# Kernel tuning notes

Measured on AMD Instinct MI355X. Metric: run time of the kernel, lower is better.

Reference implementation:

```python
import jax, jax.numpy as jnp
import numpy as np

NUM_NOD = 6
MAX_PREV = 5
NUM_EDGE = 20  # (1+5)*5//2 + 5*(6-5)
D = 1024
H = 8
LN_EPS = 1e-6


def setup_inputs() -> dict:
    key = jax.random.key(0)
    ks = jax.random.split(key, 12)
    B, S = 8, 1024
    scale = 1.0 / np.sqrt(D)
    return {
        "inputs": jax.random.normal(ks[0], (B, S, D), jnp.float32),
        "ew": jax.random.uniform(ks[1], (NUM_NOD, 3), jnp.float32),
        "act_w": jax.random.uniform(ks[2], (NUM_NOD,), jnp.float32),
        "We": jax.random.normal(ks[3], (NUM_EDGE, D, D), jnp.float32) * scale,
        "be": jnp.zeros((NUM_EDGE, D), jnp.float32),
        "Wq": jax.random.normal(ks[4], (NUM_NOD, D, D), jnp.float32) * scale,
        "Wk": jax.random.normal(ks[5], (NUM_NOD, D, D), jnp.float32) * scale,
        "Wv": jax.random.normal(ks[6], (NUM_NOD, D, D), jnp.float32) * scale,
        "Wo": jax.random.normal(ks[7], (NUM_NOD, D, D), jnp.float32) * scale,
        "ln_g": jnp.ones((D,), jnp.float32),
        "ln_b": jnp.zeros((D,), jnp.float32),
    }


def _layernorm(x, g, b):
    mu = jnp.mean(x, axis=-1, keepdims=True)
    var = jnp.mean(jnp.square(x - mu), axis=-1, keepdims=True)
    return (x - mu) * jax.lax.rsqrt(var + LN_EPS) * g + b


def _mha(q, k, v, wq, wk, wv, wo):
    B, S, d = q.shape
    dh = d // H
    qh = (q @ wq).reshape(B, S, H, dh)
    kh = (k @ wk).reshape(B, S, H, dh)
    vh = (v @ wv).reshape(B, S, H, dh)
    scores = jnp.einsum("bqhd,bkhd->bhqk", qh, kh) / jnp.sqrt(jnp.asarray(dh, q.dtype))
    attn = jax.nn.softmax(scores, axis=-1)
    ctx = jnp.einsum("bhqk,bkhd->bqhd", attn, vh).reshape(B, S, d)
    return ctx @ wo


def reference(inputs, ew, act_w, We, be, Wq, Wk, Wv, Wo, ln_g, ln_b):
    # Fixed (deterministic) routing: node act = attention (q,k,v) for all nodes.
    # Edge op = linear (sel_ope 3). q from node c-1, k from earliest visible node,
    # v from the middle of the visible window; gated by Gumbel weights ew/act_w.
    nodes = {-1: inputs}
    lind = 0
    for c in range(NUM_NOD):
        nsrc = min(c + 1, MAX_PREV)
        snode = c - nsrc
        eq, ek, ev = lind + nsrc - 1, lind, lind + nsrc // 2
        in_q, in_k, in_v = c - 1, snode, snode + nsrc // 2
        q = ew[c, 0] * (nodes[in_q] @ We[eq] + be[eq])
        k = ew[c, 1] * (nodes[in_k] @ We[ek] + be[ek])
        v = ew[c, 2] * (nodes[in_v] @ We[ev] + be[ev])
        o = _mha(q, k, v, Wq[c], Wk[c], Wv[c], Wo[c])
        nodes[c] = act_w[c] * o + q  # gated attention + residual
        lind += nsrc
    # only node 5 is unconsumed under this routing
    out = nodes[NUM_NOD - 1]
    return _layernorm(out, ln_g, ln_b)
```

## Files before the change

kernel.cpp:

```cpp
#include <hip/hip_runtime.h>
#include <stdint.h>

#define DD 1024
#define MM 8192

typedef unsigned short u16;
typedef __attribute__((ext_vector_type(8))) short s16x8;
typedef __attribute__((ext_vector_type(4))) short s16x4;
typedef __attribute__((ext_vector_type(8))) __bf16 bf16x8;
typedef __attribute__((ext_vector_type(4))) float f32x4;

__device__ inline u16 f2bf(float f) {
  uint32_t u = __builtin_bit_cast(uint32_t, f);
  u += 0x7fffu + ((u >> 16) & 1u);
  return (u16)(u >> 16);
}
__device__ inline u16 f2bf_rn(float f) {
  return __builtin_bit_cast(u16, (__bf16)f);
}
__device__ inline float bf2f(u16 h) {
  return __builtin_bit_cast(float, (uint32_t)h << 16);
}
__device__ inline f32x4 mfma32(s16x8 a, s16x8 b, f32x4 c) {
  return __builtin_amdgcn_mfma_f32_16x16x32_bf16(
      __builtin_bit_cast(bf16x8, a), __builtin_bit_cast(bf16x8, b), c, 0, 0, 0);
}

struct CvtJobs { const float* p[23]; u16* d[23]; };
__global__ __launch_bounds__(256) void k_cvtN(CvtJobs cs) {
  int z = blockIdx.y;
  const float4* p = (const float4*)cs.p[z];
  u16* out = cs.d[z];
  int i = blockIdx.x * 256 + threadIdx.x;
  float4 a = p[2 * i], b = p[2 * i + 1];
  union { s16x8 v; u16 u[8]; } r;
  r.u[0] = f2bf(a.x); r.u[1] = f2bf(a.y); r.u[2] = f2bf(a.z); r.u[3] = f2bf(a.w);
  r.u[4] = f2bf(b.x); r.u[5] = f2bf(b.y); r.u[6] = f2bf(b.z); r.u[7] = f2bf(b.w);
  ((s16x8*)out)[i] = r.v;
}

struct WSrcs { const float* p[18]; };
__global__ __launch_bounds__(256) void k_wtransN(WSrcs ws, u16* __restrict__ pool) {
  __shared__ u16 t[32][33];
  int m = blockIdx.z;
  const float* src = ws.p[m];
  u16* dst = pool + (size_t)m * DD * DD;
  int c0 = blockIdx.x * 32, r0 = blockIdx.y * 32;
  int tx = threadIdx.x, ty = threadIdx.y;
  #pragma unroll
  for (int j = 0; j < 4; ++j)
    t[ty + j * 8][tx] = f2bf(src[(size_t)(r0 + ty + j * 8) * DD + c0 + tx]);
  __syncthreads();
  #pragma unroll
  for (int j = 0; j < 4; ++j)
    dst[(size_t)(c0 + ty + j * 8) * DD + r0 + tx] = t[tx][ty + j * 8];
}

struct BiasArgs { const float* be[18]; };
__global__ __launch_bounds__(256) void k_biasN(BiasArgs ba, const u16* __restrict__ wt,
                                               float* __restrict__ outv) {
  int z = blockIdx.y, n = blockIdx.x * 256 + threadIdx.x;
  const u16* row = wt + (size_t)z * DD * DD + (size_t)n * DD;
  const float* be = ba.be[z];
  float acc = 0.0f;
  for (int k8 = 0; k8 < DD / 8; ++k8) {
    s16x8 w = *(const s16x8*)(row + k8 * 8);
    const float4* bp = (const float4*)(be + k8 * 8);
    float4 b0 = bp[0], b1 = bp[1];
    acc += b0.x * bf2f((u16)w[0]) + b0.y * bf2f((u16)w[1]) +
           b0.z * bf2f((u16)w[2]) + b0.w * bf2f((u16)w[3]) +
           b1.x * bf2f((u16)w[4]) + b1.y * bf2f((u16)w[5]) +
           b1.z * bf2f((u16)w[6]) + b1.w * bf2f((u16)w[7]);
  }
  outv[(size_t)z * DD + n] = acc;
}

struct CombArgs { const u16* a[18]; const u16* b[18]; u16* cbase; };
__global__ __launch_bounds__(256, 2) void k_gemmC(CombArgs ca) {
  const u16* A = ca.a[blockIdx.z];
  const u16* Bt = ca.b[blockIdx.z];
  u16* C = ca.cbase + (size_t)blockIdx.z * DD * DD;
  __shared__ u16 As[128 * 64];
  __shared__ u16 Bs[128 * 64];
  const int tid = threadIdx.x;
  const int lane = tid & 63, wave = tid >> 6;
  const int g = lane >> 4, r15 = lane & 15;
  const int m0 = blockIdx.x * 128, n0 = blockIdx.y * 128;
  const int wm = (wave >> 1) * 64, wn = (wave & 1) * 64;
  f32x4 acc[4][4] = {};
  for (int kt = 0; kt < 16; ++kt) {
    const int k0 = kt * 64;
    __syncthreads();
    #pragma unroll
    for (int i = 0; i < 4; ++i) {
      int c = tid + i * 256;
      int row = c >> 3, kc = (c & 7) ^ (row & 7);
      __builtin_amdgcn_global_load_lds(
          (__attribute__((address_space(1))) void*)(A + (size_t)(m0 + row) * DD + k0 + kc * 8),
          (__attribute__((address_space(3))) void*)(As + c * 8), 16, 0, 0);
    }
    #pragma unroll
    for (int i = 0; i < 4; ++i) {
      int c = tid + i * 256;
      int row = c >> 3, kc = (c & 7) ^ (row & 7);
      __builtin_amdgcn_global_load_lds(
          (__attribute__((address_space(1))) void*)(Bt + (size_t)(n0 + row) * DD + k0 + kc * 8),
          (__attribute__((address_space(3))) void*)(Bs + c * 8), 16, 0, 0);
    }
    __syncthreads();
    #pragma unroll
    for (int ks = 0; ks < 2; ++ks) {
      s16x8 af[4], bfr[4];
      #pragma unroll
      for (int f = 0; f < 4; ++f) {
        int row = wm + f * 16 + r15;
        int kc = (ks * 4 + g) ^ (row & 7);
        af[f] = *(const s16x8*)(As + row * 64 + kc * 8);
        int rowb = wn + f * 16 + r15;
        int kcb = (ks * 4 + g) ^ (rowb & 7);
        bfr[f] = *(const s16x8*)(Bs + rowb * 64 + kcb * 8);
      }
      #pragma unroll
      for (int fm = 0; fm < 4; ++fm)
        #pragma unroll
        for (int fn = 0; fn < 4; ++fn)
          acc[fm][fn] = mfma32(af[fm], bfr[fn], acc[fm][fn]);
    }
  }
  #pragma unroll
  for (int fm = 0; fm < 4; ++fm)
    #pragma unroll
    for (int fn = 0; fn < 4; ++fn) {
      int col = n0 + wn + fn * 16 + r15;
      #pragma unroll
      for (int j = 0; j < 4; ++j) {
        int row = m0 + wm + fm * 16 + g * 4 + j;
        C[(size_t)row * DD + col] = f2bf(acc[fm][fn][j]);
      }
    }
}

struct GemmJob {
  const u16* A; const u16* Bt; const float* bias; const u16* resid;
  float* f32out;
  u16* out0; const float* s0p; float s0c;
  u16* out1; const float* s1p;
  u16* out2; const float* s2p;
  u16* vtout;
};
struct GemmBatch { GemmJob j[3]; };

__global__ __launch_bounds__(256, 2) void k_gemmN(GemmBatch gb) {
  const GemmJob jb = gb.j[blockIdx.z];
  __shared__ u16 As[128 * 64];
  __shared__ u16 Bs[128 * 64];
  const int tid = threadIdx.x;
  const int lane = tid & 63, wave = tid >> 6;
  const int g = lane >> 4, r15 = lane & 15;
  const int m0 = blockIdx.x * 128, n0 = blockIdx.y * 128;
  const int wm = (wave >> 1) * 64, wn = (wave & 1) * 64;
  f32x4 acc[4][4] = {};
  for (int kt = 0; kt < 16; ++kt) {
    const int k0 = kt * 64;
    __syncthreads();
    #pragma unroll
    for (int i = 0; i < 4; ++i) {
      int c = tid + i * 256;
      int row = c >> 3, kc = (c & 7) ^ (row & 7);
      __builtin_amdgcn_global_load_lds(
          (__attribute__((address_space(1))) void*)(jb.A + (size_t)(m0 + row) * DD + k0 + kc * 8),
          (__attribute__((address_space(3))) void*)(As + c * 8), 16, 0, 0);
    }
    #pragma unroll
    for (int i = 0; i < 4; ++i) {
      int c = tid + i * 256;
      int row = c >> 3, kc = (c & 7) ^ (row & 7);
      __builtin_amdgcn_global_load_lds(
          (__attribute__((address_space(1))) void*)(jb.Bt + (size_t)(n0 + row) * DD + k0 + kc * 8),
          (__attribute__((address_space(3))) void*)(Bs + c * 8), 16, 0, 0);
    }
    __syncthreads();
    #pragma unroll
    for (int ks = 0; ks < 2; ++ks) {
      s16x8 af[4], bfr[4];
      #pragma unroll
      for (int f = 0; f < 4; ++f) {
        int row = wm + f * 16 + r15;
        int kc = (ks * 4 + g) ^ (row & 7);
        af[f] = *(const s16x8*)(As + row * 64 + kc * 8);
        int rowb = wn + f * 16 + r15;
        int kcb = (ks * 4 + g) ^ (rowb & 7);
        bfr[f] = *(const s16x8*)(Bs + rowb * 64 + kcb * 8);
      }
      #pragma unroll
      for (int fm = 0; fm < 4; ++fm)
        #pragma unroll
        for (int fn = 0; fn < 4; ++fn)
          acc[fm][fn] = mfma32(af[fm], bfr[fn], acc[fm][fn]);
    }
  }
  const float s0 = jb.s0c * (jb.s0p ? jb.s0p[0] : 1.0f);
  if (jb.vtout) {
    #pragma unroll
    for (int fm = 0; fm < 4; ++fm) {
      #pragma unroll
      for (int fn = 0; fn < 4; ++fn) {
        int col = n0 + wn + fn * 16 + r15;
        float bcol = jb.bias ? jb.bias[col] : 0.0f;
        int row0 = m0 + wm + fm * 16 + g * 4;
        int b_ = row0 >> 10, h_ = col >> 7, d_ = col & 127, s_ = row0 & 1023;
        union { s16x4 v; u16 u[4]; } q4;
        #pragma unroll
        for (int j = 0; j < 4; ++j) q4.u[j] = f2bf(s0 * (acc[fm][fn][j] + bcol));
        *(s16x4*)(jb.vtout + (((size_t)(b_ * 8 + h_) * 128 + d_) << 10) + s_) = q4.v;
      }
    }
    return;
  }
  const float s1 = (jb.s1p ? jb.s1p[0] : 1.0f);
  const float s2 = (jb.s2p ? jb.s2p[0] : 1.0f);
  #pragma unroll
  for (int fm = 0; fm < 4; ++fm) {
    #pragma unroll
    for (int fn = 0; fn < 4; ++fn) {
      int col = n0 + wn + fn * 16 + r15;
      float bcol = jb.bias ? jb.bias[col] : 0.0f;
      #pragma unroll
      for (int j = 0; j < 4; ++j) {
        int row = m0 + wm + fm * 16 + g * 4 + j;
        size_t idx = (size_t)row * DD + col;
        float v = acc[fm][fn][j] + bcol;
        float v0 = s0 * v + (jb.resid ? bf2f(jb.resid[idx]) : 0.0f);
        if (jb.out0) jb.out0[idx] = f2bf(v0);
        if (jb.f32out) jb.f32out[idx] = v0;
        if (jb.out1) jb.out1[idx] = f2bf(s1 * v);
        if (jb.out2) jb.out2[idx] = f2bf(s2 * v);
      }
    }
  }
}

__global__ __launch_bounds__(256, 2) void k_attn(
    const u16* __restrict__ qp, const u16* __restrict__ kp,
    const u16* __restrict__ vt, u16* __restrict__ ctx) {
  __shared__ u16 Ks[2][64 * 128];
  __shared__ u16 Vs[128 * 72];
  const int lin = blockIdx.y * gridDim.x + blockIdx.x;
  const int m = lin >> 3;
  const int bh = (lin & 7) * 8 + (m & 7);
  const int q0 = (m >> 3) * 128;
  const int b = bh >> 3, h = bh & 7;
  const int tid = threadIdx.x, lane = tid & 63, wave = tid >> 6;
  const int g = lane >> 4, r15 = lane & 15;
  s16x8 qf[2][4];
  #pragma unroll
  for (int qg = 0; qg < 2; ++qg) {
    const u16* qb = qp + (size_t)(b * 1024 + q0 + wave * 32 + qg * 16 + r15) * DD + h * 128;
    #pragma unroll
    for (int kk = 0; kk < 4; ++kk) qf[qg][kk] = *(const s16x8*)(qb + kk * 32 + g * 8);
  }
  f32x4 o0[8] = {}, o1[8] = {};
  float lps0 = 0.0f, lps1 = 0.0f;
  const u16* kpb = kp + (size_t)b * 1024 * DD + h * 128;
  const u16* vtb = vt + (size_t)bh * 128 * 1024;

  s16x8 vreg[4];
  auto stageK = [&](int t, int buf) {
    #pragma unroll
    for (int i = 0; i < 4; ++i) {
      int c = tid + i * 256;
      int row = c >> 4, kc = (c & 15) ^ (row & 7);
      __builtin_amdgcn_global_load_lds(
          (__attribute__((address_space(1))) void*)(kpb + (size_t)(t * 64 + row) * DD + kc * 8),
          (__attribute__((address_space(3))) void*)(Ks[buf] + c * 8), 16, 0, 0);
    }
  };
  auto loadV = [&](int t) {
    #pragma unroll
    for (int i = 0; i < 4; ++i) {
      int c = tid + i * 256;
      int row = c >> 3, kc = c & 7;
      vreg[i] = *(const s16x8*)(vtb + (size_t)row * 1024 + t * 64 + kc * 8);
    }
  };
  auto writeV = [&]() {
    #pragma unroll
    for (int i = 0; i < 4; ++i) {
      int c = tid + i * 256;
      int row = c >> 3, kc = c & 7;
      *(s16x8*)(Vs + row * 72 + kc * 8) = vreg[i];
    }
  };

  stageK(0, 0);
  loadV(0);
  writeV();
  __syncthreads();

  union pk_t { s16x8 v; u16 u[8]; };
  for (int t = 0; t < 16; ++t) {
    const int cur = t & 1;
    if (t < 15) {
      stageK(t + 1, cur ^ 1);
      loadV(t + 1);
    }
    f32x4 s0[4] = {}, s1[4] = {};
    __builtin_amdgcn_s_setprio(1);
    #pragma unroll
    for (int sub = 0; sub < 4; ++sub) {
      const int krow = sub * 16 + r15;
      #pragma unroll
      for (int kk = 0; kk < 4; ++kk) {
        int slot = (kk * 4 + g) ^ (krow & 7);
        s16x8 kf = *(const s16x8*)(Ks[cur] + krow * 128 + slot * 8);
        s0[sub] = mfma32(kf, qf[0][kk], s0[sub]);
        s1[sub] = mfma32(kf, qf[1][kk], s1[sub]);
      }
    }
    __builtin_amdgcn_s_setprio(0);
    pk_t pa0[2], pa1[2];
    #pragma unroll
    for (int sub = 0; sub < 4; ++sub)
      #pragma unroll
      for (int j = 0; j < 4; ++j) {
        float pe = exp2f(s0[sub][j] - 16.0f);
        lps0 += pe;
        pa0[sub >> 1].u[(sub & 1) * 4 + j] = f2bf_rn(pe);
      }
    #pragma unroll
    for (int sub = 0; sub < 4; ++sub)
      #pragma unroll
      for (int j = 0; j < 4; ++j) {
        float pe = exp2f(s1[sub][j] - 16.0f);
        lps1 += pe;
        pa1[sub >> 1].u[(sub & 1) * 4 + j] = f2bf_rn(pe);
      }
    __builtin_amdgcn_s_setprio(1);
    #pragma unroll
    for (int p01 = 0; p01 < 2; ++p01) {
      #pragma unroll
      for (int dt = 0; dt < 8; ++dt) {
        union { s16x8 v; s16x4 h[2]; } vv;
        const u16* vbase = Vs + (dt * 16 + r15) * 72 + p01 * 32 + g * 4;
        vv.h[0] = *(const s16x4*)(vbase);
        vv.h[1] = *(const s16x4*)(vbase + 16);
        o0[dt] = mfma32(pa0[p01].v, vv.v, o0[dt]);
        o1[dt] = mfma32(pa1[p01].v, vv.v, o1[dt]);
      }
    }
    __builtin_amdgcn_s_setprio(0);
    __syncthreads();
    if (t < 15) {
      writeV();
      __syncthreads();
    }
  }
  lps0 += __shfl_xor(lps0, 16);
  lps0 += __shfl_xor(lps0, 32);
  lps1 += __shfl_xor(lps1, 16);
  lps1 += __shfl_xor(lps1, 32);
  {
    float inv = 1.0f / lps0;
    #pragma unroll
    for (int j = 0; j < 4; ++j) {
      float cj = __shfl(inv, (lane & 48) + g * 4 + j);
      size_t row = (size_t)(b * 1024 + q0 + wave * 32 + g * 4 + j);
      #pragma unroll
      for (int dt = 0; dt < 8; ++dt)
        ctx[row * DD + h * 128 + dt * 16 + r15] = f2bf(o0[dt][j] * cj);
    }
  }
  {
    float inv = 1.0f / lps1;
    #pragma unroll
    for (int j = 0; j < 4; ++j) {
      float cj = __shfl(inv, (lane & 48) + g * 4 + j);
      size_t row = (size_t)(b * 1024 + q0 + wave * 32 + 16 + g * 4 + j);
      #pragma unroll
      for (int dt = 0; dt < 8; ++dt)
        ctx[row * DD + h * 128 + dt * 16 + r15] = f2bf(o1[dt][j] * cj);
    }
  }
}

__global__ __launch_bounds__(256) void k_ln(const float* __restrict__ x,
                                            const float* __restrict__ gam,
                                            const float* __restrict__ bet,
                                            float* __restrict__ out) {
  __shared__ float red[8];
  const int row = blockIdx.x, tid = threadIdx.x, lane = tid & 63, wave = tid >> 6;
  const float4 v = ((const float4*)(x + (size_t)row * DD))[tid];
  float s = v.x + v.y + v.z + v.w;
  #pragma unroll
  for (int m = 1; m < 64; m <<= 1) s += __shfl_xor(s, m);
  if (lane == 0) red[wave] = s;
  __syncthreads();
  float mu = (red[0] + red[1] + red[2] + red[3]) * (1.0f / DD);
  float dx = v.x - mu, dy = v.y - mu, dz = v.z - mu, dw = v.w - mu;
  float q = dx * dx + dy * dy + dz * dz + dw * dw;
  #pragma unroll
  for (int m = 1; m < 64; m <<= 1) q += __shfl_xor(q, m);
  if (lane == 0) red[wave + 4] = q;
  __syncthreads();
  float var = (red[4] + red[5] + red[6] + red[7]) * (1.0f / DD);
  float inv = rsqrtf(var + 1e-6f);
  const float4 gv = ((const float4*)gam)[tid];
  const float4 bv = ((const float4*)bet)[tid];
  float4 r;
  r.x = dx * inv * gv.x + bv.x;
  r.y = dy * inv * gv.y + bv.y;
  r.z = dz * inv * gv.z + bv.z;
  r.w = dw * inv * gv.w + bv.w;
  ((float4*)(out + (size_t)row * DD))[tid] = r;
}

extern "C" void kernel_launch(void* const* d_in, const int* in_sizes, int n_in,
                              void* d_out, int out_size, void* d_ws, size_t ws_size,
                              hipStream_t stream) {
  const float* inputs = (const float*)d_in[0];
  const float* ew     = (const float*)d_in[1];
  const float* act_w  = (const float*)d_in[2];
  const float* We     = (const float*)d_in[3];
  const float* be     = (const float*)d_in[4];
  const float* Wq     = (const float*)d_in[5];
  const float* Wk     = (const float*)d_in[6];
  const float* Wv     = (const float*)d_in[7];
  const float* Wo     = (const float*)d_in[8];
  const float* ln_g   = (const float*)d_in[9];
  const float* ln_b   = (const float*)d_in[10];
  float* out = (float*)d_out;

  uint8_t* w = (uint8_t*)d_ws;
  size_t off = 0;
  auto alloc = [&](size_t bytes) {
    uint8_t* p = w + off;
    off += (bytes + 255) & ~(size_t)255;
    return p;
  };
  const size_t XB = (size_t)MM * DD * 2;
  const size_t WB = (size_t)DD * DD * 2;
  const size_t XBu = (size_t)MM * DD;
  const size_t WBu = (size_t)DD * DD;

  u16* Xbuf[5];
  for (int i = 0; i < 5; ++i) Xbuf[i] = (u16*)alloc(XB);
  u16* Comb  = (u16*)alloc(18 * WB);
  u16* rot   = (u16*)alloc(4 * WB);
  float* biasv = (float*)alloc(18 * DD * 4);
  u16* S     = (u16*)alloc(5 * XB);
  if (off > ws_size) {
    (void)hipMemsetAsync(d_out, 0x7F, (size_t)out_size * 4, stream);
    return;
  }
  u16* Xb[6] = {Xbuf[0], Xbuf[1], Xbuf[2], Xbuf[3], Xbuf[4], Xbuf[0]};
  u16* qb = S, * ctxb = S + XBu, * qpb = S + 2 * XBu, * kpb = S + 3 * XBu,
     * vtb = S + 4 * XBu;
  float* n5 = (float*)qpb;
  u16* stP = S;
  u16* stW = S + 18 * WBu;

  struct Node { int sq, eq, sk, ek, sv, ev; };
  static const Node route[6] = {
      {-1, 0, -1, 0, -1, 0},
      {0, 2, -1, 1, 0, 2},
      {1, 5, -1, 3, 0, 4},
      {2, 9, -1, 6, 1, 8},
      {3, 14, -1, 10, 1, 12},
      {4, 19, 0, 15, 2, 17},
  };
  const float QS = 1.4426950408889634f * 0.088388347648318433f;

  int emap[20]; for (int i = 0; i < 20; ++i) emap[i] = -1;
  int uniq[20]; int nu = 0;
  for (int c = 0; c < 6; ++c) {
    int es[3] = {route[c].eq, route[c].ek, route[c].ev};
    for (int t = 0; t < 3; ++t)
      if (emap[es[t]] < 0) { emap[es[t]] = nu; uniq[nu++] = es[t]; }
  }

  CvtJobs cv;
  for (int j = 0; j < nu; ++j) { cv.p[j] = We + (size_t)uniq[j] * WBu; cv.d[j] = stW + (size_t)j * WBu; }
  for (int j = 0; j < 8; ++j)  { cv.p[nu + j] = inputs + (size_t)j * WBu; cv.d[nu + j] = Xb[0] + (size_t)j * WBu; }
  k_cvtN<<<dim3(512, nu + 8), 256, 0, stream>>>(cv);
  WSrcs w18;
  for (int c = 0; c < 6; ++c) {
    w18.p[c * 3 + 0] = Wq + (size_t)c * WBu;
    w18.p[c * 3 + 1] = Wk + (size_t)c * WBu;
    w18.p[c * 3 + 2] = Wv + (size_t)c * WBu;
  }
  k_wtransN<<<dim3(32, 32, 18), dim3(32, 8), 0, stream>>>(w18, stP);
  CombArgs ca;
  BiasArgs ba;
  for (int c = 0; c < 6; ++c) {
    int es[3] = {route[c].eq, route[c].ek, route[c].ev};
    for (int t = 0; t < 3; ++t) {
      int i = c * 3 + t;
      ca.a[i] = stP + (size_t)i * WBu;
      ca.b[i] = stW + (size_t)emap[es[t]] * WBu;
      ba.be[i] = be + (size_t)es[t] * DD;
    }
  }
  ca.cbase = Comb;
  k_gemmC<<<dim3(8, 8, 18), 256, 0, stream>>>(ca);
  k_biasN<<<dim3(4, 18), 256, 0, stream>>>(ba, stP, biasv);

  GemmJob oprojPrev{};
  for (int c = 0; c < 6; ++c) {
    const Node& nd = route[c];
    u16* qeT = rot + (size_t)(c & 1) * 2 * WBu;
    u16* WoT = qeT + WBu;

    GemmJob kap = {Xb[nd.sk + 1], Comb + (size_t)(c * 3 + 1) * WBu,
                   biasv + (size_t)(c * 3 + 1) * DD, nullptr, nullptr,
                   kpb, ew + 3 * c + 1, 1.0f,
                   nullptr, nullptr, nullptr, nullptr, nullptr};
    GemmJob vap = {Xb[nd.sv + 1], Comb + (size_t)(c * 3 + 2) * WBu,
                   biasv + (size_t)(c * 3 + 2) * DD, nullptr, nullptr,
                   nullptr, ew + 3 * c + 2, 1.0f,
                   nullptr, nullptr, nullptr, nullptr, vtb};
    GemmJob qed = {Xb[nd.sq + 1], qeT, be + (size_t)nd.eq * DD, nullptr, nullptr,
                   qb, ew + 3 * c + 0, 1.0f,
                   nullptr, nullptr, nullptr, nullptr, nullptr};
    GemmJob qap = {Xb[nd.sq + 1], Comb + (size_t)(c * 3 + 0) * WBu,
                   biasv + (size_t)(c * 3 + 0) * DD, nullptr, nullptr,
                   qpb, ew + 3 * c + 0, QS,
                   nullptr, nullptr, nullptr, nullptr, nullptr};

    GemmBatch A{};
    int za = 0;
    if (c >= 1) A.j[za++] = oprojPrev;
    A.j[za++] = kap;
    if (c != 1) A.j[za++] = vap;
    k_gemmN<<<dim3(64, 8, za), 256, 0, stream>>>(A);

    if ((c & 1) == 0) {
      WSrcs w4{};
      w4.p[0] = We + (size_t)route[c].eq * WBu;
      w4.p[1] = Wo + (size_t)c * WBu;
      w4.p[2] = We + (size_t)route[c + 1].eq * WBu;
      w4.p[3] = Wo + (size_t)(c + 1) * WBu;
      k_wtransN<<<dim3(32, 32, 4), dim3(32, 8), 0, stream>>>(w4, rot);
    }

    GemmBatch B{};
    int zb = 0;
    if (c == 1) B.j[zb++] = vap;
    B.j[zb++] = qed;
    B.j[zb++] = qap;
    k_gemmN<<<dim3(64, 8, zb), 256, 0, stream>>>(B);

    k_attn<<<dim3(8, 64), 256, 0, stream>>>(qpb, kpb, vtb, ctxb);

    oprojPrev = GemmJob{ctxb, WoT, nullptr, qb,
                        (c == 5) ? n5 : nullptr,
                        (c < 5) ? Xb[c + 1] : nullptr, act_w + c, 1.0f,
                        nullptr, nullptr, nullptr, nullptr, nullptr};
  }
  GemmBatch F{};
  F.j[0] = oprojPrev;
  k_gemmN<<<dim3(64, 8, 1), 256, 0, stream>>>(F);
  k_ln<<<dim3(MM), 256, 0, stream>>>(n5, ln_g, ln_b, out);
}
```

Before: 1.127 ms.

## Double-buffer V tile via direct global-to-LDS loads with XOR swizzle

The attention kernel's V tile was loaded into registers and written to a padded LDS buffer after compute, which cost an extra barrier per iteration. It now uses async global_load_lds into a double-buffered, XOR-swizzled V buffer, the same scheme already used for K. This removes the register staging, the extra writeback and one __syncthreads per step. In exchange LDS use rises by 8 KB per block, which could limit occupancy, and the swizzled reads need extra index arithmetic.

```diff
diff --git a/kernel.cpp b/kernel.cpp
--- a/kernel.cpp
+++ b/kernel.cpp
@@ -244,7 +244,7 @@
     const u16* __restrict__ qp, const u16* __restrict__ kp,
     const u16* __restrict__ vt, u16* __restrict__ ctx) {
   __shared__ u16 Ks[2][64 * 128];
-  __shared__ u16 Vs[128 * 72];
+  __shared__ u16 Vs[2][128 * 64];
   const int lin = blockIdx.y * gridDim.x + blockIdx.x;
   const int m = lin >> 3;
   const int bh = (lin & 7) * 8 + (m & 7);
@@ -264,7 +264,6 @@
   const u16* kpb = kp + (size_t)b * 1024 * DD + h * 128;
   const u16* vtb = vt + (size_t)bh * 128 * 1024;
 
-  s16x8 vreg[4];
   auto stageK = [&](int t, int buf) {
     #pragma unroll
     for (int i = 0; i < 4; ++i) {
@@ -275,26 +274,19 @@
           (__attribute__((address_space(3))) void*)(Ks[buf] + c * 8), 16, 0, 0);
     }
   };
-  auto loadV = [&](int t) {
+  auto stageV = [&](int t, int buf) {
     #pragma unroll
     for (int i = 0; i < 4; ++i) {
       int c = tid + i * 256;
-      int row = c >> 3, kc = c & 7;
-      vreg[i] = *(const s16x8*)(vtb + (size_t)row * 1024 + t * 64 + kc * 8);
+      int row = c >> 3, gch = (c & 7) ^ (row & 7);
+      __builtin_amdgcn_global_load_lds(
+          (__attribute__((address_space(1))) void*)(vtb + (size_t)row * 1024 + t * 64 + gch * 8),
+          (__attribute__((address_space(3))) void*)(Vs[buf] + c * 8), 16, 0, 0);
     }
   };
-  auto writeV = [&]() {
-    #pragma unroll
-    for (int i = 0; i < 4; ++i) {
-      int c = tid + i * 256;
-      int row = c >> 3, kc = c & 7;
-      *(s16x8*)(Vs + row * 72 + kc * 8) = vreg[i];
-    }
-  };
 
   stageK(0, 0);
-  loadV(0);
-  writeV();
+  stageV(0, 0);
   __syncthreads();
 
   union pk_t { s16x8 v; u16 u[8]; };
@@ -302,7 +294,7 @@
     const int cur = t & 1;
     if (t < 15) {
       stageK(t + 1, cur ^ 1);
-      loadV(t + 1);
+      stageV(t + 1, cur ^ 1);
     }
     f32x4 s0[4] = {}, s1[4] = {};
     __builtin_amdgcn_s_setprio(1);
@@ -338,22 +330,19 @@
     __builtin_amdgcn_s_setprio(1);
     #pragma unroll
     for (int p01 = 0; p01 < 2; ++p01) {
+      const int ch0 = p01 * 4 + (g >> 1), off = (g & 1) * 4;
       #pragma unroll
       for (int dt = 0; dt < 8; ++dt) {
-        union { s16x8 v; s16x4 h[2]; } vv;
-        const u16* vbase = Vs + (dt * 16 + r15) * 72 + p01 * 32 + g * 4;
-        vv.h[0] = *(const s16x4*)(vbase);
-        vv.h[1] = *(const s16x4*)(vbase + 16);
+        const int row = dt * 16 + r15, rx = row & 7;
+        union { s16x8 v; s16x4 hh[2]; } vv;
+        vv.hh[0] = *(const s16x4*)(Vs[cur] + row * 64 + ((ch0 ^ rx) * 8 + off));
+        vv.hh[1] = *(const s16x4*)(Vs[cur] + row * 64 + (((ch0 + 2) ^ rx) * 8 + off));
         o0[dt] = mfma32(pa0[p01].v, vv.v, o0[dt]);
         o1[dt] = mfma32(pa1[p01].v, vv.v, o1[dt]);
       }
     }
     __builtin_amdgcn_s_setprio(0);
     __syncthreads();
-    if (t < 15) {
-      writeV();
-      __syncthreads();
-    }
   }
   lps0 += __shfl_xor(lps0, 16);
   lps0 += __shfl_xor(lps0, 32);
```

New measurement: 1.130 ms. About the same (+0.2%).
